# Kernel tuning notes

Hardware: AMD Instinct MI355X
Metric: run time of the kernel (lower is better)

## Reference

```python
import jax, jax.numpy as jnp
import numpy as np

HIDDEN = 512

def setup_inputs() -> dict:
    key = jax.random.key(0)
    k1, k2, k3, k4 = jax.random.split(key, 4)
    B, T, H = 64, 4096, HIDDEN
    hidden = jax.random.normal(k1, (B, H), dtype=jnp.float32)
    encoder_outputs = jax.random.normal(k2, (B, T, H), dtype=jnp.float32)
    # nn.Linear(H, H) parameters: weight [H, H], bias [H]
    lim = 1.0 / np.sqrt(H)
    W = jax.random.uniform(k3, (H, H), minval=-lim, maxval=lim, dtype=jnp.float32)
    b = jax.random.uniform(k4, (H,), minval=-lim, maxval=lim, dtype=jnp.float32)
    return {"hidden": hidden, "encoder_outputs": encoder_outputs, "W": W, "b": b}

def reference(hidden, encoder_outputs, W, b):
    # method == 'general': energy[b,t] = dot(Linear(encoder_outputs[b,t]), hidden[b])
    # projected: [B, T, H] = enc @ W.T + b
    proj = jnp.einsum('bth,oh->bto', encoder_outputs, W) + b
    scores = jnp.einsum('bth,bh->bt', proj, hidden)  # [B, T]
    attn = jax.nn.softmax(scores, axis=1)            # row softmax over time
    return attn[:, None, :]                           # [B, 1, T]
```

## Files before the change

### kernel.cpp

```cpp
#include <hip/hip_runtime.h>
#include <math.h>

#define HID 512
#define TLEN 4096
#define BATCH 64

__global__ __launch_bounds__(HID) void proj_kernel(const float* __restrict__ hidden,
                                                   const float* __restrict__ W,
                                                   float* __restrict__ v) {
    __shared__ float hs[HID];
    const int b = blockIdx.x;
    const int h = threadIdx.x;
    hs[h] = hidden[b * HID + h];
    __syncthreads();
    float s = 0.f;
#pragma unroll 16
    for (int o = 0; o < HID; ++o) {
        s = fmaf(hs[o], W[o * HID + h], s);
    }
    v[b * HID + h] = s;
}

__global__ __launch_bounds__(256) void score_kernel(const float* __restrict__ enc,
                                                    const float* __restrict__ v,
                                                    float* __restrict__ scores) {
    __shared__ float4 vs[HID / 4];
    const int b    = blockIdx.y;
    const int tid  = threadIdx.x;
    const int wave = tid >> 6;
    const int lane = tid & 63;
    const int g    = lane >> 3;
    const int j    = lane & 7;

    if (tid < HID / 4) vs[tid] = ((const float4*)(v + b * HID))[tid];
    __syncthreads();

    const float4* e4 = (const float4*)(enc + (size_t)b * TLEN * HID);
    const int rowBase = blockIdx.x * 128 + wave * 32;

#pragma unroll
    for (int batch = 0; batch < 4; ++batch) {
        const int t = rowBase + batch * 8 + g;
        const float4* row = e4 + (size_t)t * (HID / 4);
        float s0 = 0.f, s1 = 0.f;
#pragma unroll
        for (int k = 0; k < 16; k += 2) {
            const float4 a0 = row[k * 8 + j];
            const float4 a1 = row[(k + 1) * 8 + j];
            const float4 v0 = vs[k * 8 + j];
            const float4 v1 = vs[(k + 1) * 8 + j];
            s0 += a0.x * v0.x + a0.y * v0.y + a0.z * v0.z + a0.w * v0.w;
            s1 += a1.x * v1.x + a1.y * v1.y + a1.z * v1.z + a1.w * v1.w;
        }
        float s = s0 + s1;
        s += __shfl_xor(s, 1, 64);
        s += __shfl_xor(s, 2, 64);
        s += __shfl_xor(s, 4, 64);
        if (j == 0) scores[b * TLEN + t] = s;
    }
}

__global__ __launch_bounds__(1024) void softmax_kernel(const float* __restrict__ scores,
                                                       float* __restrict__ out) {
    __shared__ float redm[16];
    __shared__ float reds[16];
    const int b    = blockIdx.x;
    const int tid  = threadIdx.x;
    const int wave = tid >> 6;
    const int lane = tid & 63;

    const float4 x = ((const float4*)(scores + b * TLEN))[tid];

    float m = fmaxf(fmaxf(x.x, x.y), fmaxf(x.z, x.w));
#pragma unroll
    for (int off = 32; off; off >>= 1) m = fmaxf(m, __shfl_xor(m, off, 64));
    if (lane == 0) redm[wave] = m;
    __syncthreads();
    if (wave == 0) {
        float t = (lane < 16) ? redm[lane] : -INFINITY;
#pragma unroll
        for (int off = 8; off; off >>= 1) t = fmaxf(t, __shfl_xor(t, off, 64));
        if (lane == 0) redm[0] = t;
    }
    __syncthreads();
    m = redm[0];

    float4 e;
    e.x = __expf(x.x - m);
    e.y = __expf(x.y - m);
    e.z = __expf(x.z - m);
    e.w = __expf(x.w - m);
    float sum = e.x + e.y + e.z + e.w;
#pragma unroll
    for (int off = 32; off; off >>= 1) sum += __shfl_xor(sum, off, 64);
    if (lane == 0) reds[wave] = sum;
    __syncthreads();
    if (wave == 0) {
        float t = (lane < 16) ? reds[lane] : 0.f;
#pragma unroll
        for (int off = 8; off; off >>= 1) t += __shfl_xor(t, off, 64);
        if (lane == 0) reds[0] = t;
    }
    __syncthreads();
    const float inv = 1.0f / reds[0];

    float4 o4;
    o4.x = e.x * inv; o4.y = e.y * inv; o4.z = e.z * inv; o4.w = e.w * inv;
    ((float4*)(out + b * TLEN))[tid] = o4;
}

extern "C" void kernel_launch(void* const* d_in, const int* in_sizes, int n_in,
                              void* d_out, int out_size, void* d_ws, size_t ws_size,
                              hipStream_t stream) {
    const float* hidden = (const float*)d_in[0];
    const float* enc    = (const float*)d_in[1];
    const float* W      = (const float*)d_in[2];
    float* out = (float*)d_out;

    float* v      = (float*)d_ws;
    float* scores = v + BATCH * HID;

    proj_kernel<<<dim3(BATCH), dim3(HID), 0, stream>>>(hidden, W, v);
    score_kernel<<<dim3(TLEN / 128, BATCH), dim3(256), 0, stream>>>(enc, v, scores);
    softmax_kernel<<<dim3(BATCH), dim3(1024), 0, stream>>>(scores, out);
}
```

Baseline: 702.8 us.

## Double-buffer encoder tiles into LDS via async global_load_lds in score kernel

Rewrites the score kernel so each block streams 512 time rows through two LDS tile buffers. Tiles are filled with the asynchronous global_load_lds builtin, so the next tile is fetched while the current one is dotted against v. The row mapping changes to 16 lanes per row with a 4-step shuffle reduction. The grid shrinks to 8 blocks per batch. This trades parallelism and occupancy, from larger LDS use and fewer blocks, for deeper memory prefetching, and adds a barrier per tile.

```diff
diff --git a/kernel.cpp b/kernel.cpp
--- a/kernel.cpp
+++ b/kernel.cpp
@@ -4,6 +4,14 @@
 #define HID 512
 #define TLEN 4096
 #define BATCH 64
+
+#define TILE_ROWS 16
+#define ROWS_PER_BLOCK 512
+#define TILES_PER_BLOCK (ROWS_PER_BLOCK / TILE_ROWS)
+#define TILE_F4 (TILE_ROWS * HID / 4)
+
+#define GLOBAL_AS __attribute__((address_space(1)))
+#define LDS_AS    __attribute__((address_space(3)))
 
 __global__ __launch_bounds__(HID) void proj_kernel(const float* __restrict__ hidden,
                                                    const float* __restrict__ W,
@@ -25,38 +33,55 @@
                                                     const float* __restrict__ v,
                                                     float* __restrict__ scores) {
     __shared__ float4 vs[HID / 4];
+    __shared__ float4 buf[2][TILE_F4];
+
     const int b    = blockIdx.y;
+    const int bx   = blockIdx.x;
     const int tid  = threadIdx.x;
-    const int wave = tid >> 6;
+    const int w    = tid >> 6;
     const int lane = tid & 63;
-    const int g    = lane >> 3;
-    const int j    = lane & 7;
+    const int g    = lane >> 4;
+    const int j    = lane & 15;
 
     if (tid < HID / 4) vs[tid] = ((const float4*)(v + b * HID))[tid];
+
+    const float4* encT = (const float4*)enc
+                       + ((size_t)b * TLEN + (size_t)bx * ROWS_PER_BLOCK) * (HID / 4);
+
+    auto stage = [&](int T) {
+        const float4* gsrc = encT + (size_t)T * TILE_F4 + w * 512 + lane;
+        float4* ldst = &buf[T & 1][w * 512];
+#pragma unroll
+        for (int i = 0; i < 8; ++i) {
+            __builtin_amdgcn_global_load_lds(
+                (GLOBAL_AS const void*)(gsrc + i * 64),
+                (LDS_AS void*)(ldst + i * 64),
+                16, 0, 0);
+        }
+    };
+
+    stage(0);
     __syncthreads();
 
-    const float4* e4 = (const float4*)(enc + (size_t)b * TLEN * HID);
-    const int rowBase = blockIdx.x * 128 + wave * 32;
+    for (int T = 0; T < TILES_PER_BLOCK; ++T) {
+        if (T + 1 < TILES_PER_BLOCK) stage(T + 1);
 
+        const float4* src = &buf[T & 1][(w * 4 + g) * (HID / 4)];
+        float acc = 0.f;
 #pragma unroll
-    for (int batch = 0; batch < 4; ++batch) {
-        const int t = rowBase + batch * 8 + g;
-        const float4* row = e4 + (size_t)t * (HID / 4);
-        float s0 = 0.f, s1 = 0.f;
-#pragma unroll
-        for (int k = 0; k < 16; k += 2) {
-            const float4 a0 = row[k * 8 + j];
-            const float4 a1 = row[(k + 1) * 8 + j];
-            const float4 v0 = vs[k * 8 + j];
-            const float4 v1 = vs[(k + 1) * 8 + j];
-            s0 += a0.x * v0.x + a0.y * v0.y + a0.z * v0.z + a0.w * v0.w;
-            s1 += a1.x * v1.x + a1.y * v1.y + a1.z * v1.z + a1.w * v1.w;
+        for (int k = 0; k < 8; ++k) {
+            const float4 e  = src[k * 16 + j];
+            const float4 vv = vs[k * 16 + j];
+            acc += e.x * vv.x + e.y * vv.y + e.z * vv.z + e.w * vv.w;
         }
-        float s = s0 + s1;
-        s += __shfl_xor(s, 1, 64);
-        s += __shfl_xor(s, 2, 64);
-        s += __shfl_xor(s, 4, 64);
-        if (j == 0) scores[b * TLEN + t] = s;
+        acc += __shfl_xor(acc, 1, 64);
+        acc += __shfl_xor(acc, 2, 64);
+        acc += __shfl_xor(acc, 4, 64);
+        acc += __shfl_xor(acc, 8, 64);
+        if (j == 0)
+            scores[b * TLEN + bx * ROWS_PER_BLOCK + T * TILE_ROWS + w * 4 + g] = acc;
+
+        __syncthreads();
     }
 }
 
@@ -121,6 +146,6 @@
     float* scores = v + BATCH * HID;
 
     proj_kernel<<<dim3(BATCH), dim3(HID), 0, stream>>>(hidden, W, v);
-    score_kernel<<<dim3(TLEN / 128, BATCH), dim3(256), 0, stream>>>(enc, v, scores);
+    score_kernel<<<dim3(TLEN / ROWS_PER_BLOCK, BATCH), dim3(256), 0, stream>>>(enc, v, scores);
     softmax_kernel<<<dim3(BATCH), dim3(1024), 0, stream>>>(scores, out);
 }
```

After: 699.8 us. About the same (-0.4%).
